# Kernel optimization log

Measured on AMD Instinct MI355X. Metric: run time of the kernel, lower is better.

Reference implementation:

```python
import jax, jax.numpy as jnp
import numpy as np

WS = 32  # window size hardcoded in the original module

def _dwconv7(x, w, b):
    # x: (B,C,H,W), w: (C,1,7,7) depthwise
    y = jax.lax.conv_general_dilated(
        x, w, window_strides=(1, 1), padding='SAME',
        dimension_numbers=('NCHW', 'OIHW', 'NCHW'),
        feature_group_count=x.shape[1])
    return y + b[None, :, None, None]


def setup_inputs() -> dict:
    key = jax.random.key(0)
    ks = jax.random.split(key, 9)
    B, C, H, W = 4, 64, 128, 128
    x = jax.random.normal(ks[0], (B, C, H, W), dtype=jnp.float32)
    s = 0.05
    conv1_w = jax.random.normal(ks[1], (C, 1, 7, 7), dtype=jnp.float32) * s
    conv1_b = jax.random.normal(ks[2], (C,), dtype=jnp.float32) * s
    conv2_w = jax.random.normal(ks[3], (C, C), dtype=jnp.float32) * s
    conv2_b = jax.random.normal(ks[4], (C,), dtype=jnp.float32) * s
    conv3_w = jax.random.normal(ks[5], (C, C), dtype=jnp.float32) * s
    conv3_b = jax.random.normal(ks[6], (C,), dtype=jnp.float32) * s
    conv4_w = jax.random.normal(ks[7], (C, C), dtype=jnp.float32) * s
    conv4_b = jax.random.normal(ks[8], (C,), dtype=jnp.float32) * s
    return {'x': x, 'conv1_w': conv1_w, 'conv1_b': conv1_b,
            'conv2_w': conv2_w, 'conv2_b': conv2_b,
            'conv3_w': conv3_w, 'conv3_b': conv3_b,
            'conv4_w': conv4_w, 'conv4_b': conv4_b}


def reference(x, conv1_w, conv1_b, conv2_w, conv2_b, conv3_w, conv3_b, conv4_w, conv4_b):
    B, C, H, W = x.shape
    scale = jnp.asarray(C, x.dtype) ** -0.5
    h = _dwconv7(x, conv1_w, conv1_b)
    # window partition: (B,C,H,W) -> (N, C, WS*WS) with N = B*(H/WS)*(W/WS)
    hw = h.reshape(B, C, H // WS, WS, W // WS, WS)
    hw = hw.transpose(0, 2, 4, 1, 3, 5).reshape(-1, C, WS * WS)  # (N,C,P)
    # 1x1 convs as channel matmuls
    q = jnp.einsum('oc,ncp->nop', conv2_w, hw) + conv2_b[None, :, None]  # (N,C,P)
    k = jnp.einsum('oc,ncp->nop', conv3_w, hw) + conv3_b[None, :, None]  # (N,C,P)
    # att = k^T @ q * scale, softmax over dim 1 (first spatial axis)
    att = jnp.einsum('ncp,ncq->npq', k, q) * scale  # (N,P,P)
    att = jax.nn.softmax(att, axis=1)
    out = jnp.einsum('ncp,npq->ncq', hw, att)  # (N,C,P)
    out = jnp.einsum('oc,ncq->noq', conv4_w, out) + conv4_b[None, :, None]
    # un-partition back to (B,C,H,W)
    out = out.reshape(B, H // WS, W // WS, C, WS, WS)
    out = out.transpose(0, 3, 1, 4, 2, 5).reshape(B, C, H, W)
    return out
```

## Files before the change

### kernel.cpp

```cpp
#include <hip/hip_runtime.h>

typedef unsigned int  u32;
typedef unsigned short u16;
typedef short s16x8 __attribute__((ext_vector_type(8)));
typedef float f32x16 __attribute__((ext_vector_type(16)));

#define BB   4
#define CC   64
#define HH   128
#define WW   128
#define NWIN 64
#define PP   1024

__device__ __forceinline__ u16 f2bf(float f) {
  u32 x = __float_as_uint(f);
  return (u16)((x + 0x7fffu + ((x >> 16) & 1u)) >> 16);
}
__device__ __forceinline__ u32 pk2(float a, float b) {
  return (u32)f2bf(a) | ((u32)f2bf(b) << 16);
}

__global__ __launch_bounds__(256)
void dwconv_kernel(const float* __restrict__ x, const float* __restrict__ w,
                   const float* __restrict__ bias, float* __restrict__ hw,
                   u16* __restrict__ vb, float* __restrict__ vsum) {
  int blk = blockIdx.x;
  int n = blk >> 6, c = blk & 63;
  int b = n >> 4, wy = (n >> 2) & 3, wx = n & 3;
  int y0 = wy * 32 - 3, x0 = wx * 32 - 3;
  __shared__ float patch[38][40];
  __shared__ float wf[49];
  __shared__ float wsum[4];
  int tid = threadIdx.x;
  if (tid < 49) wf[tid] = w[c * 49 + tid];
  const float* xp = x + (size_t)(b * CC + c) * HH * WW;
  for (int i = tid; i < 38 * 38; i += 256) {
    int py = i / 38, px = i - py * 38;
    int gy = y0 + py, gx = x0 + px;
    float v = 0.f;
    if (gy >= 0 && gy < HH && gx >= 0 && gx < WW) v = xp[gy * WW + gx];
    patch[py][px] = v;
  }
  __syncthreads();
  float bv = bias[c];
  int yy = tid >> 3;
  int xg = (tid & 7) << 2;
  float o0_ = bv, o1_ = bv, o2_ = bv, o3_ = bv;
  #pragma unroll
  for (int dy = 0; dy < 7; ++dy) {
    const float* pr = &patch[yy + dy][xg];
    float4 ra = *(const float4*)pr;
    float4 rb = *(const float4*)(pr + 4);
    float4 rc = *(const float4*)(pr + 8);
    float rv[12] = {ra.x, ra.y, ra.z, ra.w, rb.x, rb.y, rb.z, rb.w,
                    rc.x, rc.y, rc.z, rc.w};
    #pragma unroll
    for (int dx = 0; dx < 7; ++dx) {
      float wgt = wf[dy * 7 + dx];
      o0_ = fmaf(rv[dx],     wgt, o0_);
      o1_ = fmaf(rv[dx + 1], wgt, o1_);
      o2_ = fmaf(rv[dx + 2], wgt, o2_);
      o3_ = fmaf(rv[dx + 3], wgt, o3_);
    }
  }
  size_t obase = (size_t)(n * CC + c) * PP + yy * 32 + xg;
  *(float4*)(hw + obase) = make_float4(o0_, o1_, o2_, o3_);
  *(uint2*)(vb + obase) = make_uint2(pk2(o0_, o1_), pk2(o2_, o3_));
  float psum = (o0_ + o1_) + (o2_ + o3_);
  #pragma unroll
  for (int off = 1; off < 64; off <<= 1) psum += __shfl_xor(psum, off);
  if ((tid & 63) == 0) wsum[tid >> 6] = psum;
  __syncthreads();
  if (tid == 0) vsum[blk] = (wsum[0] + wsum[1]) + (wsum[2] + wsum[3]);
}

__global__ __launch_bounds__(256)
void qk_kernel(const float* __restrict__ hw,
               const float* __restrict__ w2, const float* __restrict__ b2,
               const float* __restrict__ w3, const float* __restrict__ b3,
               u16* __restrict__ qT, u16* __restrict__ kT) {
  int n = blockIdx.x >> 4;
  int chunk = blockIdx.x & 15;
  int tid = threadIdx.x;
  int lane = tid & 63, wvi = tid >> 6;
  int l31 = lane & 31, hi = lane >> 5;
  int phalf = wvi & 1, ochalf = wvi >> 1;
  int p0 = (chunk << 6) + (phalf << 5);
  int oc0 = ochalf << 5;

  union FU { u32 u[4]; s16x8 v; };

  s16x8 bq[4], bk[4];
  {
    const float* w2r = w2 + (oc0 + l31) * 64 + (hi << 3);
    const float* w3r = w3 + (oc0 + l31) * 64 + (hi << 3);
    #pragma unroll
    for (int kst = 0; kst < 4; ++kst) {
      float4 a = *(const float4*)(w2r + kst * 16);
      float4 b = *(const float4*)(w2r + kst * 16 + 4);
      FU f;
      f.u[0] = pk2(a.x * 0.125f, a.y * 0.125f);
      f.u[1] = pk2(a.z * 0.125f, a.w * 0.125f);
      f.u[2] = pk2(b.x * 0.125f, b.y * 0.125f);
      f.u[3] = pk2(b.z * 0.125f, b.w * 0.125f);
      bq[kst] = f.v;
      float4 c = *(const float4*)(w3r + kst * 16);
      float4 d = *(const float4*)(w3r + kst * 16 + 4);
      f.u[0] = pk2(c.x, c.y); f.u[1] = pk2(c.z, c.w);
      f.u[2] = pk2(d.x, d.y); f.u[3] = pk2(d.z, d.w);
      bk[kst] = f.v;
    }
  }

  f32x16 accq, acck;
  #pragma unroll
  for (int j = 0; j < 16; ++j) { accq[j] = 0.f; acck[j] = 0.f; }

  const float* hbase = hw + ((size_t)n << 16) + (size_t)(hi << 3) * PP
                       + p0 + l31;
  #pragma unroll
  for (int kst = 0; kst < 4; ++kst) {
    const float* hp = hbase + (size_t)(kst * 16) * PP;
    float h[8];
    #pragma unroll
    for (int e = 0; e < 8; ++e) h[e] = hp[e * PP];
    FU fh, fl;
    #pragma unroll
    for (int t = 0; t < 4; ++t) {
      u32 ph;
      asm("v_cvt_pk_bf16_f32 %0, %1, %2"
          : "=v"(ph) : "v"(h[2 * t]), "v"(h[2 * t + 1]));
      fh.u[t] = ph;
      float r0 = h[2 * t]     - __uint_as_float(ph << 16);
      float r1 = h[2 * t + 1] - __uint_as_float(ph & 0xffff0000u);
      u32 pl;
      asm("v_cvt_pk_bf16_f32 %0, %1, %2" : "=v"(pl) : "v"(r0), "v"(r1));
      fl.u[t] = pl;
    }
    accq = __builtin_amdgcn_mfma_f32_32x32x16_bf16(fh.v, bq[kst], accq, 0, 0, 0);
    accq = __builtin_amdgcn_mfma_f32_32x32x16_bf16(fl.v, bq[kst], accq, 0, 0, 0);
    acck = __builtin_amdgcn_mfma_f32_32x32x16_bf16(fh.v, bk[kst], acck, 0, 0, 0);
    acck = __builtin_amdgcn_mfma_f32_32x32x16_bf16(fl.v, bk[kst], acck, 0, 0, 0);
  }

  float biasq = b2[oc0 + l31] * 0.125f;
  float biask = b3[oc0 + l31];
  u16* qrow = qT + (((size_t)n << 10) + p0) * 64 + oc0 + l31;
  u16* krow = kT + (((size_t)n << 10) + p0) * 64 + oc0 + l31;
  #pragma unroll
  for (int r = 0; r < 16; ++r) {
    int pr = (r & 3) + ((r >> 2) << 3) + (hi << 2);
    qrow[pr * 64] = f2bf(accq[r] + biasq);
    krow[pr * 64] = f2bf(acck[r] + biask);
  }
}

__global__ __launch_bounds__(256)
void attn_kernel(const u16* __restrict__ qT, const u16* __restrict__ kT,
                 const u16* __restrict__ vB, const float* __restrict__ vsum,
                 const float* __restrict__ w4, const float* __restrict__ b4,
                 float* __restrict__ outp) {
  int bid = blockIdx.x;
  int w = (bid & 7) * 64 + (bid >> 3);
  int n = w >> 3, qb = w & 7;
  int tid = threadIdx.x;

  __shared__ __align__(16) unsigned char KsB[2][8192];
  __shared__ __align__(16) unsigned char VsB[2][8192];
  __shared__ __align__(16) unsigned char Osm[16384];
  __shared__ float l_inv[4][32];

  int lane = tid & 63, wv = tid >> 6;
  int l31 = lane & 31, hi = lane >> 5;
  int sz = (lane & 7) << 4;
  int hi16 = hi << 4;

  const size_t nbase = (size_t)n << 16;
  const u16* kg = kT + nbase;
  const u16* vg = vB + nbase;

  s16x8 qf[4];
  {
    const u16* qp = qT + nbase
                    + (size_t)((qb << 7) + (wv << 5) + l31) * 64 + (hi << 3);
    #pragma unroll
    for (int kc = 0; kc < 4; ++kc) qf[kc] = *(const s16x8*)(qp + kc * 16);
  }

  int i0 = tid, i1 = tid + 256;
  int row0 = i0 >> 3, c80 = i0 & 7;
  int row1 = i1 >> 3, c81 = i1 & 7;
  int dst0 = row0 * 128 + ((c80 * 16) ^ ((row0 & 7) << 4));
  int dst1 = row1 * 128 + ((c81 * 16) ^ ((row1 & 7) << 4));
  const u16* ks0 = kg + (size_t)row0 * 64 + c80 * 8;
  const u16* ks1 = kg + (size_t)row1 * 64 + c81 * 8;
  const u16* vs0 = vg + (size_t)row0 * 1024 + c80 * 8;
  const u16* vs1 = vg + (size_t)row1 * 1024 + c81 * 8;

  {
    uint4 ka = *(const uint4*)ks0;
    uint4 kb = *(const uint4*)ks1;
    uint4 va = *(const uint4*)vs0;
    uint4 vbx = *(const uint4*)vs1;
    *(uint4*)(KsB[0] + dst0) = ka;
    *(uint4*)(KsB[0] + dst1) = kb;
    *(uint4*)(VsB[0] + dst0) = va;
    *(uint4*)(VsB[0] + dst1) = vbx;
  }
  __syncthreads();

  f32x16 o0, o1;
  #pragma unroll
  for (int j = 0; j < 16; ++j) { o0[j] = 0.f; o1[j] = 0.f; }
  float lsum = 0.f;

  int cur = 0;
  for (int pt = 0; pt < 16; ++pt) {
    uint4 ka, kb, va, vbx;
    if (pt < 15) {
      size_t pn = (size_t)((pt + 1) << 6);
      ka  = *(const uint4*)(ks0 + pn * 64);
      kb  = *(const uint4*)(ks1 + pn * 64);
      va  = *(const uint4*)(vs0 + pn);
      vbx = *(const uint4*)(vs1 + pn);
    }

    const unsigned char* Kc = KsB[cur];
    const unsigned char* Vc = VsB[cur];

    f32x16 s0, s1;
    #pragma unroll
    for (int j = 0; j < 16; ++j) { s0[j] = 0.f; s1[j] = 0.f; }
    #pragma unroll
    for (int kc = 0; kc < 4; ++kc) {
      int cb = kc * 32 + hi16;
      s16x8 a0 = *(const s16x8*)(Kc + l31 * 128 + (cb ^ sz));
      s16x8 a1 = *(const s16x8*)(Kc + (32 + l31) * 128 + (cb ^ sz));
      s0 = __builtin_amdgcn_mfma_f32_32x32x16_bf16(a0, qf[kc], s0, 0, 0, 0);
      s1 = __builtin_amdgcn_mfma_f32_32x32x16_bf16(a1, qf[kc], s1, 0, 0, 0);
    }

    #pragma unroll
    for (int j = 0; j < 16; ++j) {
      float e = __expf(s0[j]); lsum += e; s0[j] = e - 1.0f;
    }
    #pragma unroll
    for (int j = 0; j < 16; ++j) {
      float e = __expf(s1[j]); lsum += e; s1[j] = e - 1.0f;
    }

    u32 t0,t1,t2,t3,t4,t5,t6,t7, u0,u1,u2,u3,u4,u5,u6,u7;
#define CVT(d, a, b) asm("v_cvt_pk_bf16_f32 %0, %1, %2" : "=v"(d) : "v"(a), "v"(b))
#define SWP(a, b)    asm("v_permlane32_swap_b32 %0, %1" : "+v"(a), "+v"(b))
    CVT(t0, s0[0],  s0[1]);  CVT(t1, s0[2],  s0[3]);
    CVT(t2, s0[4],  s0[5]);  CVT(t3, s0[6],  s0[7]);
    CVT(t4, s0[8],  s0[9]);  CVT(t5, s0[10], s0[11]);
    CVT(t6, s0[12], s0[13]); CVT(t7, s0[14], s0[15]);
    SWP(t0, t2); SWP(t1, t3); SWP(t4, t6); SWP(t5, t7);
    CVT(u0, s1[0],  s1[1]);  CVT(u1, s1[2],  s1[3]);
    CVT(u2, s1[4],  s1[5]);  CVT(u3, s1[6],  s1[7]);
    CVT(u4, s1[8],  s1[9]);  CVT(u5, s1[10], s1[11]);
    CVT(u6, s1[12], s1[13]); CVT(u7, s1[14], s1[15]);
    SWP(u0, u2); SWP(u1, u3); SWP(u4, u6); SWP(u5, u7);
#undef CVT
#undef SWP
    union FU { u32 u[4]; s16x8 v; };
    FU fA; fA.u[0]=t0; fA.u[1]=t1; fA.u[2]=t2; fA.u[3]=t3;
    FU fB; fB.u[0]=t4; fB.u[1]=t5; fB.u[2]=t6; fB.u[3]=t7;
    FU fC; fC.u[0]=u0; fC.u[1]=u1; fC.u[2]=u2; fC.u[3]=u3;
    FU fD; fD.u[0]=u4; fD.u[1]=u5; fD.u[2]=u6; fD.u[3]=u7;

#define PV_STEP(frag, pb) do { \
      s16x8 bv0 = *(const s16x8*)(Vc + l31 * 128 + ((pb) ^ sz)); \
      s16x8 bv1 = *(const s16x8*)(Vc + (32 + l31) * 128 + ((pb) ^ sz)); \
      o0 = __builtin_amdgcn_mfma_f32_32x32x16_bf16(frag, bv0, o0, 0, 0, 0); \
      o1 = __builtin_amdgcn_mfma_f32_32x32x16_bf16(frag, bv1, o1, 0, 0, 0); \
    } while (0)
    PV_STEP(fA.v, 0 + hi16);
    PV_STEP(fB.v, 32 + hi16);
    PV_STEP(fC.v, 64 + hi16);
    PV_STEP(fD.v, 96 + hi16);
#undef PV_STEP

    if (pt < 15) {
      *(uint4*)(KsB[cur ^ 1] + dst0) = ka;
      *(uint4*)(KsB[cur ^ 1] + dst1) = kb;
      *(uint4*)(VsB[cur ^ 1] + dst0) = va;
      *(uint4*)(VsB[cur ^ 1] + dst1) = vbx;
      __syncthreads();
      cur ^= 1;
    }
  }

  lsum += __shfl_xor(lsum, 32);
  if (hi == 0) l_inv[wv][l31] = 1.0f / lsum;

  float vsa = vsum[(n << 6) + l31];
  float vsb = vsum[(n << 6) + 32 + l31];
  int g0 = l31 >> 3, g1 = (32 + l31) >> 3;
  int bi = (l31 & 7) << 1;
  #pragma unroll
  for (int r = 0; r < 16; ++r) {
    int qr = (r & 3) + ((r >> 2) << 3) + (hi << 2);
    int row = (wv << 5) + qr;
    float li = l_inv[wv][qr];
    int rs = (row & 7) << 4;
    *(u16*)(Osm + row * 128 + ((g0 << 4) ^ rs) + bi) = f2bf((vsa + o0[r]) * li);
    *(u16*)(Osm + row * 128 + ((g1 << 4) ^ rs) + bi) = f2bf((vsb + o1[r]) * li);
  }

  union FU2 { u32 u[4]; s16x8 v; };
  int orow = (wv << 5) + l31;
  int osw = (orow & 7) << 4;
  s16x8 bf[4];
  #pragma unroll
  for (int kst = 0; kst < 4; ++kst)
    bf[kst] = *(const s16x8*)(Osm + orow * 128 + ((((kst << 1) + hi) << 4) ^ osw));

  f32x16 d2a, d2b;
  #pragma unroll
  for (int j = 0; j < 16; ++j) { d2a[j] = 0.f; d2b[j] = 0.f; }
  {
    const float* w4r = w4 + l31 * 64 + (hi << 3);
    #pragma unroll
    for (int kst = 0; kst < 4; ++kst) {
      float4 a = *(const float4*)(w4r + kst * 16);
      float4 b = *(const float4*)(w4r + kst * 16 + 4);
      FU2 f;
      f.u[0] = pk2(a.x, a.y); f.u[1] = pk2(a.z, a.w);
      f.u[2] = pk2(b.x, b.y); f.u[3] = pk2(b.z, b.w);
      d2a = __builtin_amdgcn_mfma_f32_32x32x16_bf16(f.v, bf[kst], d2a, 0, 0, 0);
    }
    const float* w4r2 = w4 + (32 + l31) * 64 + (hi << 3);
    #pragma unroll
    for (int kst = 0; kst < 4; ++kst) {
      float4 a = *(const float4*)(w4r2 + kst * 16);
      float4 b = *(const float4*)(w4r2 + kst * 16 + 4);
      FU2 f;
      f.u[0] = pk2(a.x, a.y); f.u[1] = pk2(a.z, a.w);
      f.u[2] = pk2(b.x, b.y); f.u[3] = pk2(b.z, b.w);
      d2b = __builtin_amdgcn_mfma_f32_32x32x16_bf16(f.v, bf[kst], d2b, 0, 0, 0);
    }
  }

  int b_ = n >> 4, wy = (n >> 2) & 3, wx = n & 3;
  int y = wy * 32 + (qb << 2) + wv;
  int x = wx * 32 + l31;
  float* obase = outp + ((size_t)b_ * CC * HH + y) * WW + x;
  #pragma unroll
  for (int r = 0; r < 16; ++r) {
    int ocr = (r & 3) + ((r >> 2) << 3) + (hi << 2);
    obase[(size_t)ocr * HH * WW]        = d2a[r] + b4[ocr];
    obase[(size_t)(32 + ocr) * HH * WW] = d2b[r] + b4[32 + ocr];
  }
}

extern "C" void kernel_launch(void* const* d_in, const int* in_sizes, int n_in,
                              void* d_out, int out_size, void* d_ws, size_t ws_size,
                              hipStream_t stream) {
  const float* x  = (const float*)d_in[0];
  const float* w1 = (const float*)d_in[1];
  const float* b1 = (const float*)d_in[2];
  const float* w2 = (const float*)d_in[3];
  const float* b2 = (const float*)d_in[4];
  const float* w3 = (const float*)d_in[5];
  const float* b3 = (const float*)d_in[6];
  const float* w4 = (const float*)d_in[7];
  const float* b4 = (const float*)d_in[8];
  float* outp = (float*)d_out;

  char* wsb = (char*)d_ws;
  float* hw   = (float*)wsb;
  u16*   qT   = (u16*)(wsb + (16u << 20));
  u16*   kT   = (u16*)(wsb + (24u << 20));
  u16*   vb   = (u16*)(wsb + (32u << 20));
  float* vsum = (float*)(wsb + (40u << 20));

  dwconv_kernel<<<NWIN * CC, 256, 0, stream>>>(x, w1, b1, hw, vb, vsum);
  qk_kernel   <<<NWIN * 16, 256, 0, stream>>>(hw, w2, b2, w3, b3, qT, kT);
  attn_kernel <<<NWIN * 8,  256, 0, stream>>>(qT, kT, vb, vsum, w4, b4, outp);
}
```

Baseline: 145.2 us.

## Restructure depthwise conv to one channel per wave with 4x4 register tiles

The depthwise 7x7 conv kernel now assigns one channel-window to each wavefront instead of one per 256-thread block. Each lane computes a 4x4 output tile, reusing each loaded patch row across up to four output rows, and holds the 49 weights in registers. Block-level syncs and the shared-memory reduction are dropped, since each wave syncs and reduces on its own, and the grid shrinks by 4x. In exchange, register pressure rises (49 weights plus 16 accumulators) and there are fewer blocks in flight.

```diff
diff --git a/kernel.cpp b/kernel.cpp
--- a/kernel.cpp
+++ b/kernel.cpp
@@ -24,54 +24,82 @@
 void dwconv_kernel(const float* __restrict__ x, const float* __restrict__ w,
                    const float* __restrict__ bias, float* __restrict__ hw,
                    u16* __restrict__ vb, float* __restrict__ vsum) {
+  __shared__ float patch[4][38][40];
+  __shared__ float wfs[4][52];
+  int tid = threadIdx.x;
+  int lane = tid & 63, wv = tid >> 6;
   int blk = blockIdx.x;
-  int n = blk >> 6, c = blk & 63;
+  int n = blk >> 4, c = ((blk & 15) << 2) + wv;
   int b = n >> 4, wy = (n >> 2) & 3, wx = n & 3;
   int y0 = wy * 32 - 3, x0 = wx * 32 - 3;
-  __shared__ float patch[38][40];
-  __shared__ float wf[49];
-  __shared__ float wsum[4];
-  int tid = threadIdx.x;
-  if (tid < 49) wf[tid] = w[c * 49 + tid];
+
+  if (lane < 49) wfs[wv][lane] = w[c * 49 + lane];
+
   const float* xp = x + (size_t)(b * CC + c) * HH * WW;
-  for (int i = tid; i < 38 * 38; i += 256) {
+  for (int i = lane; i < 38 * 38; i += 64) {
     int py = i / 38, px = i - py * 38;
     int gy = y0 + py, gx = x0 + px;
     float v = 0.f;
     if (gy >= 0 && gy < HH && gx >= 0 && gx < WW) v = xp[gy * WW + gx];
-    patch[py][px] = v;
-  }
-  __syncthreads();
+    patch[wv][py][px] = v;
+  }
+
+  float wreg[49];
+  #pragma unroll
+  for (int t = 0; t < 12; ++t) {
+    float4 v4 = *(const float4*)&wfs[wv][t * 4];
+    wreg[t * 4] = v4.x; wreg[t * 4 + 1] = v4.y;
+    wreg[t * 4 + 2] = v4.z; wreg[t * 4 + 3] = v4.w;
+  }
+  wreg[48] = wfs[wv][48];
+
+  int tx = lane & 7, ty = lane >> 3;
   float bv = bias[c];
-  int yy = tid >> 3;
-  int xg = (tid & 7) << 2;
-  float o0_ = bv, o1_ = bv, o2_ = bv, o3_ = bv;
-  #pragma unroll
-  for (int dy = 0; dy < 7; ++dy) {
-    const float* pr = &patch[yy + dy][xg];
+  float acc[4][4];
+  #pragma unroll
+  for (int yi = 0; yi < 4; ++yi)
+    #pragma unroll
+    for (int xi = 0; xi < 4; ++xi) acc[yi][xi] = bv;
+
+  #pragma unroll
+  for (int rr = 0; rr < 10; ++rr) {
+    const float* pr = &patch[wv][ty * 4 + rr][tx * 4];
     float4 ra = *(const float4*)pr;
     float4 rb = *(const float4*)(pr + 4);
     float4 rc = *(const float4*)(pr + 8);
     float rv[12] = {ra.x, ra.y, ra.z, ra.w, rb.x, rb.y, rb.z, rb.w,
                     rc.x, rc.y, rc.z, rc.w};
     #pragma unroll
-    for (int dx = 0; dx < 7; ++dx) {
-      float wgt = wf[dy * 7 + dx];
-      o0_ = fmaf(rv[dx],     wgt, o0_);
-      o1_ = fmaf(rv[dx + 1], wgt, o1_);
-      o2_ = fmaf(rv[dx + 2], wgt, o2_);
-      o3_ = fmaf(rv[dx + 3], wgt, o3_);
-    }
-  }
-  size_t obase = (size_t)(n * CC + c) * PP + yy * 32 + xg;
-  *(float4*)(hw + obase) = make_float4(o0_, o1_, o2_, o3_);
-  *(uint2*)(vb + obase) = make_uint2(pk2(o0_, o1_), pk2(o2_, o3_));
-  float psum = (o0_ + o1_) + (o2_ + o3_);
+    for (int yi = 0; yi < 4; ++yi) {
+      if (rr >= yi && rr <= yi + 6) {
+        int dy = rr - yi;
+        #pragma unroll
+        for (int dx = 0; dx < 7; ++dx) {
+          float wgt = wreg[dy * 7 + dx];
+          acc[yi][0] = fmaf(rv[dx],     wgt, acc[yi][0]);
+          acc[yi][1] = fmaf(rv[dx + 1], wgt, acc[yi][1]);
+          acc[yi][2] = fmaf(rv[dx + 2], wgt, acc[yi][2]);
+          acc[yi][3] = fmaf(rv[dx + 3], wgt, acc[yi][3]);
+        }
+      }
+    }
+  }
+
+  size_t obase = (size_t)(n * CC + c) * PP;
+  float psum = 0.f;
+  #pragma unroll
+  for (int yi = 0; yi < 4; ++yi) {
+    int oy = ty * 4 + yi;
+    size_t off = obase + oy * 32 + tx * 4;
+    *(float4*)(hw + off) = make_float4(acc[yi][0], acc[yi][1],
+                                       acc[yi][2], acc[yi][3]);
+    *(uint2*)(vb + off) = make_uint2(pk2(acc[yi][0], acc[yi][1]),
+                                     pk2(acc[yi][2], acc[yi][3]));
+    psum += (acc[yi][0] + acc[yi][1]) + (acc[yi][2] + acc[yi][3]);
+  }
   #pragma unroll
   for (int off = 1; off < 64; off <<= 1) psum += __shfl_xor(psum, off);
-  if ((tid & 63) == 0) wsum[tid >> 6] = psum;
-  __syncthreads();
-  if (tid == 0) vsum[blk] = (wsum[0] + wsum[1]) + (wsum[2] + wsum[3]);
+  if (lane == 0) vsum[n * CC + c] = psum;
 }
 
 __global__ __launch_bounds__(256)
@@ -376,7 +404,7 @@
   u16*   vb   = (u16*)(wsb + (32u << 20));
   float* vsum = (float*)(wsb + (40u << 20));
 
-  dwconv_kernel<<<NWIN * CC, 256, 0, stream>>>(x, w1, b1, hw, vb, vsum);
+  dwconv_kernel<<<NWIN * 16, 256, 0, stream>>>(x, w1, b1, hw, vb, vsum);
   qk_kernel   <<<NWIN * 16, 256, 0, stream>>>(hw, w2, b2, w3, b3, qT, kT);
   attn_kernel <<<NWIN * 8,  256, 0, stream>>>(qT, kT, vb, vsum, w4, b4, outp);
 }
```

Result: faster. 139.9 us (-3.6%).
